# Kernel optimization log

Hardware: AMD Instinct MI355X
Metric: run time of the kernel (lower is better)

The kernel has to match this reference:

```python
import jax, jax.numpy as jnp
import numpy as np
import math

N = 131072   # number of points
C = 32       # embed_dim
K = 19       # num_class
ZD = 16      # z_dim
BN_EPS = 1e-4
SIG_THR = 0.8


def setup_inputs():
    key = jax.random.key(0)
    ks = jax.random.split(key, 16)
    f32 = jnp.float32
    rn = lambda k, s, sc=1.0: jax.random.normal(k, s, dtype=f32) * sc
    return {
        'feat': rn(ks[0], (N, C)),
        'scene_flow': rn(ks[1], (N, 3)),
        'coarse_pred': rn(ks[2], (N, K)),
        'z': rn(ks[3], (ZD,)),
        'select_w1': rn(ks[4], (C, C), 0.2),
        'bn_gamma': jnp.ones((C,), f32),
        'bn_beta': jnp.zeros((C,), f32),
        'bn_mean': jnp.zeros((C,), f32),
        'bn_var': jnp.ones((C,), f32),
        'select_w2': rn(ks[5], (C, 1), 0.2),
        'select_b2': jnp.zeros((1,), f32),
        'wq': rn(ks[6], (C, C), 0.2), 'bq': jnp.zeros((C,), f32),
        'wk': rn(ks[7], (C, C), 0.2), 'bk': jnp.zeros((C,), f32),
        'wv': rn(ks[8], (C, C), 0.2), 'bv': jnp.zeros((C,), f32),
        'wo': rn(ks[9], (C, C), 0.2), 'bo': jnp.zeros((C,), f32),
        'wt': rn(ks[10], (2 * C, C), 0.2), 'bt': jnp.zeros((C,), f32),
        'w_out': rn(ks[11], (C, K), 0.2), 'b_out': jnp.zeros((K,), f32),
        'w_gen': rn(ks[12], (ZD + K + 3, C), 0.2), 'b_gen': jnp.zeros((C,), f32),
    }


def _forward(feat, scene_flow, coarse_pred, z, select_w1, bn_gamma, bn_beta,
             bn_mean, bn_var, select_w2, select_b2, wq, bq, wk, bk, wv, bv,
             wo, bo, wt, bt, w_out, b_out, w_gen, b_gen):
    cp = jax.nn.softmax(coarse_pred, axis=-1)                      # (N, K)
    temp_mask = jnp.any(scene_flow != 0, axis=-1)                  # (N,)
    # select_mlp: Linear(no bias) -> BatchNorm(eval, eps=1e-4) -> ReLU -> Linear -> Sigmoid
    h = (feat @ select_w1 - bn_mean) / jnp.sqrt(bn_var + BN_EPS) * bn_gamma + bn_beta
    h = jnp.maximum(h, 0.0)
    score = jax.nn.sigmoid(h @ select_w2 + select_b2)[:, 0]        # (N,)
    valid = (score < SIG_THR) & temp_mask                          # (N,)
    # cvae stand-in: linear over concat(z, onehot(class), scene_flow) -> (N, K, C)
    wz, wc, ws = w_gen[:ZD], w_gen[ZD:ZD + K], w_gen[ZD + K:]
    gen = (z @ wz + b_gen)[None, None, :] + wc[None, :, :] + (scene_flow @ ws)[:, None, :]
    gen = gen * cp[:, :, None]                                     # scale by softmax prob
    # tiny cross-attention: 1 query per point over K=19 class prototypes
    q = feat @ wq + bq                                             # (N, C)
    k_ = jnp.einsum('nkc,cd->nkd', gen, wk) + bk                   # (N, K, C)
    v_ = jnp.einsum('nkc,cd->nkd', gen, wv) + bv                   # (N, K, C)
    attn = jax.nn.softmax(jnp.einsum('nd,nkd->nk', q, k_) / math.sqrt(C), axis=-1)
    aug = jnp.einsum('nk,nkd->nd', attn, v_) @ wo + bo             # (N, C)
    # scatter-back: invalid points get zeros (equivalent to torch boolean scatter)
    new_feat = jnp.where(valid[:, None], aug, 0.0)
    refine = jnp.concatenate([feat, new_feat], axis=-1) @ wt + bt  # (N, C)
    return refine @ w_out + b_out                                  # (N, K)


def reference(feat, scene_flow, coarse_pred, z, select_w1, bn_gamma, bn_beta,
              bn_mean, bn_var, select_w2, select_b2, wq, bq, wk, bk, wv, bv,
              wo, bo, wt, bt, w_out, b_out, w_gen, b_gen):
    return _forward(feat, scene_flow, coarse_pred, z, select_w1, bn_gamma,
                    bn_beta, bn_mean, bn_var, select_w2, select_b2, wq, bq,
                    wk, bk, wv, bv, wo, bo, wt, bt, w_out, b_out, w_gen, b_gen)
```

## Files before the change

kernel.cpp:

```cpp
#include <hip/hip_runtime.h>

#define NPTS 131072

constexpr int OFF_SW1 = 0;
constexpr int OFF_BNS = 1024;
constexpr int OFF_BNH = 1056;
constexpr int OFF_SW2 = 1088;
constexpr int OFF_B2  = 1120;
constexpr int OFF_QG  = 1121;
constexpr int OFF_QGB = 1729;
constexpr int OFF_QM  = 1748;
constexpr int OFF_QMB = 1844;
constexpr int OFF_QBV = 1847;
constexpr int OFF_QBB = 1879;
constexpr int OFF_A1  = 1880;
constexpr int OFF_GVB = 2488;
constexpr int OFF_MVB = 2849;
constexpr int OFF_CV  = 2906;
constexpr int OFF_BB  = 2925;
constexpr int XG   = 3072;
constexpr int XA2  = 3680;
constexpr int XMK  = 4288;
constexpr int XMV  = 4384;
constexpr int XGK  = 4480;
constexpr int XGV  = 5088;
constexpr int XB   = 5696;

#define CONST_AS __attribute__((address_space(4)))
__device__ __forceinline__ const CONST_AS float* to_const(const float* p) {
    return (const CONST_AS float*)p;
}

__global__ __launch_bounds__(256) void pre_a(
    const float* __restrict__ z,
    const float* __restrict__ sw1,
    const float* __restrict__ bn_gamma, const float* __restrict__ bn_beta,
    const float* __restrict__ bn_mean,  const float* __restrict__ bn_var,
    const float* __restrict__ sw2,      const float* __restrict__ sb2,
    const float* __restrict__ wq, const float* __restrict__ bq,
    const float* __restrict__ wk, const float* __restrict__ bk,
    const float* __restrict__ wv,
    const float* __restrict__ wt, const float* __restrict__ bt,
    const float* __restrict__ wout, const float* __restrict__ bout,
    const float* __restrict__ wgen, const float* __restrict__ bgen,
    float* __restrict__ W)
{
    int i = blockIdx.x * 256 + threadIdx.x;
    if (i < 1024) {
        W[OFF_SW1 + i] = sw1[(i & 31) * 32 + (i >> 5)];
    } else if (i < 1632) {
        int t = i - 1024, e = t / 19, j = t % 19;
        float a1 = 0.f, a2 = 0.f;
        for (int d = 0; d < 32; ++d) {
            float w_ = wout[d*19 + j];
            a1 += wt[e*32 + d] * w_;
            a2 += wt[(32 + e)*32 + d] * w_;
        }
        W[OFF_A1 + t] = a1; W[XA2 + t] = a2;
    } else if (i < 2240) {
        int t = i - 1632, k = t >> 5, e = t & 31;
        float g = bgen[e];
        for (int d = 0; d < 16; ++d) g += z[d] * wgen[d*32 + e];
        W[XG + t] = g + wgen[(16 + k)*32 + e];
    } else if (i < 2336) {
        int t = i - 2240, m = t >> 5, c = t & 31;
        float a = 0.f, b = 0.f;
        for (int e = 0; e < 32; ++e) {
            float wsr = wgen[(35 + m)*32 + e];
            a += wsr * wk[e*32 + c];
            b += wsr * wv[e*32 + c];
        }
        W[XMK + t] = a; W[XMV + t] = b;
    } else if (i < 2368) {
        int t = i - 2336;
        float scale = bn_gamma[t] / sqrtf(bn_var[t] + 1e-4f);
        W[OFF_BNS + t] = scale;
        W[OFF_BNH + t] = bn_beta[t] - bn_mean[t] * scale;
        W[OFF_SW2 + t] = sw2[t];
    } else if (i < 2387) {
        int t = i - 2368;
        float a = bout[t];
        for (int d = 0; d < 32; ++d) a += bt[d] * wout[d*19 + t];
        W[OFF_BB + t] = a;
    } else if (i < 2419) {
        int t = i - 2387;
        float a = 0.f;
        for (int c = 0; c < 32; ++c) a += wq[t*32 + c] * bk[c];
        W[OFF_QBV + t] = a;
    } else if (i == 2419) {
        W[OFF_B2] = sb2[0];
    } else if (i == 2420) {
        float a = 0.f;
        for (int c = 0; c < 32; ++c) a += bq[c] * bk[c];
        W[OFF_QBB] = a;
    }
}

__global__ __launch_bounds__(256) void pre_b(
    const float* __restrict__ wq, const float* __restrict__ bq,
    const float* __restrict__ wk, const float* __restrict__ wv,
    const float* __restrict__ wo,
    float* __restrict__ W)
{
    int i = blockIdx.x * 256 + threadIdx.x;
    if (i < 608) {
        int k = i >> 5, c = i & 31;
        float a = 0.f, b = 0.f;
        for (int e = 0; e < 32; ++e) {
            float g = W[XG + k*32 + e];
            a += g * wk[e*32 + c];
            b += g * wv[e*32 + c];
        }
        W[XGK + i] = a; W[XGV + i] = b;
    } else if (i < 1216) {
        int t = i - 608, c = t / 19, j = t % 19;
        float a = 0.f;
        for (int d = 0; d < 32; ++d) a += wo[c*32 + d] * W[XA2 + d*19 + j];
        W[XB + t] = a;
    } else if (i < 1312) {
        int t = i - 1216, e = t / 3, m = t % 3;
        float a = 0.f;
        for (int c = 0; c < 32; ++c) a += wq[e*32 + c] * W[XMK + m*32 + c];
        W[OFF_QM + t] = a;
    } else if (i < 1315) {
        int m = i - 1312;
        float a = 0.f;
        for (int c = 0; c < 32; ++c) a += bq[c] * W[XMK + m*32 + c];
        W[OFF_QMB + m] = a;
    }
}

__global__ __launch_bounds__(256) void pre_c(
    const float* __restrict__ wq, const float* __restrict__ bq,
    const float* __restrict__ bv, const float* __restrict__ bo,
    float* __restrict__ W)
{
    int i = blockIdx.x * 256 + threadIdx.x;
    if (i < 608) {
        int e = i / 19, k = i % 19;
        float a = 0.f;
        for (int c = 0; c < 32; ++c) a += wq[e*32 + c] * W[XGK + k*32 + c];
        W[OFF_QG + i] = a;
    } else if (i < 627) {
        int k = i - 608;
        float a = 0.f;
        for (int c = 0; c < 32; ++c) a += bq[c] * W[XGK + k*32 + c];
        W[OFF_QGB + k] = a;
    } else if (i < 988) {
        int t = i - 627, k = t / 19, j = t % 19;
        float a = 0.f;
        for (int c = 0; c < 32; ++c) a += W[XGV + k*32 + c] * W[XB + c*19 + j];
        W[OFF_GVB + t] = a;
    } else if (i < 1045) {
        int t = i - 988, m = t / 19, j = t % 19;
        float a = 0.f;
        for (int c = 0; c < 32; ++c) a += W[XMV + m*32 + c] * W[XB + c*19 + j];
        W[OFF_MVB + t] = a;
    } else if (i < 1064) {
        int j = i - 1045;
        float a = 0.f;
        for (int c = 0; c < 32; ++c) a += bv[c] * W[XB + c*19 + j];
        for (int d = 0; d < 32; ++d) a += bo[d] * W[XA2 + d*19 + j];
        W[OFF_CV + j] = a;
    }
}

__global__ __launch_bounds__(256, 1) void main_k(
    const float* __restrict__ feat,
    const float* __restrict__ sflow,
    const float* __restrict__ cpred,
    const float* __restrict__ Wg,
    float* __restrict__ out)
{
    const CONST_AS float* W = to_const(Wg);
    const int n = blockIdx.x * 256 + threadIdx.x;

    float f[32];
    const float4* fp = (const float4*)(feat + (long)n * 32);
#pragma unroll
    for (int g = 0; g < 8; ++g) {
        float4 v = fp[g];
        f[g*4+0] = v.x; f[g*4+1] = v.y; f[g*4+2] = v.z; f[g*4+3] = v.w;
    }

    float s0 = sflow[(long)n*3 + 0];
    float s1 = sflow[(long)n*3 + 1];
    float s2 = sflow[(long)n*3 + 2];
    bool tmask = (s0 != 0.f) | (s1 != 0.f) | (s2 != 0.f);

    float cp[19];
#pragma unroll
    for (int k = 0; k < 19; ++k) cp[k] = cpred[(long)n*19 + k];
    float m1 = cp[0];
#pragma unroll
    for (int k = 1; k < 19; ++k) m1 = fmaxf(m1, cp[k]);
    float sum1 = 0.f;
#pragma unroll
    for (int k = 0; k < 19; ++k) { cp[k] = __expf(cp[k] - m1); sum1 += cp[k]; }
    float r1 = 1.f / sum1;
#pragma unroll
    for (int k = 0; k < 19; ++k) cp[k] *= r1;

    float sacc = W[OFF_B2];
#pragma unroll
    for (int c = 0; c < 32; ++c) {
        float a = 0.f;
#pragma unroll
        for (int e = 0; e < 32; ++e) a = fmaf(f[e], W[OFF_SW1 + c*32 + e], a);
        float h = fmaf(a, W[OFF_BNS + c], W[OFF_BNH + c]);
        h = fmaxf(h, 0.f);
        sacc = fmaf(h, W[OFF_SW2 + c], sacc);
    }
    bool valid = tmask && (sacc < 1.3862943611198906f);

    float qg[19];
#pragma unroll
    for (int k = 0; k < 19; ++k) qg[k] = W[OFF_QGB + k];
    float qm0 = W[OFF_QMB + 0], qm1 = W[OFF_QMB + 1], qm2 = W[OFF_QMB + 2];
    float qb = W[OFF_QBB];
#pragma unroll
    for (int e = 0; e < 32; ++e) {
        float fe = f[e];
#pragma unroll
        for (int k = 0; k < 19; ++k) qg[k] = fmaf(fe, W[OFF_QG + e*19 + k], qg[k]);
        qm0 = fmaf(fe, W[OFF_QM + e*3 + 0], qm0);
        qm1 = fmaf(fe, W[OFF_QM + e*3 + 1], qm1);
        qm2 = fmaf(fe, W[OFF_QM + e*3 + 2], qm2);
        qb  = fmaf(fe, W[OFF_QBV + e], qb);
    }
    float qs = s0*qm0 + s1*qm1 + s2*qm2;

    const float RS = 0.17677669529663687f;
    float l[19];
#pragma unroll
    for (int k = 0; k < 19; ++k) l[k] = fmaf(cp[k], qg[k] + qs, qb) * RS;

    float m2 = l[0];
#pragma unroll
    for (int k = 1; k < 19; ++k) m2 = fmaxf(m2, l[k]);
    float sum2 = 0.f;
#pragma unroll
    for (int k = 0; k < 19; ++k) { l[k] = __expf(l[k] - m2); sum2 += l[k]; }
    float r2 = 1.f / sum2;
    float Sw = 0.f;
#pragma unroll
    for (int k = 0; k < 19; ++k) { l[k] = l[k] * r2 * cp[k]; Sw += l[k]; }

    float o[19];
#pragma unroll
    for (int j = 0; j < 19; ++j) o[j] = W[OFF_BB + j];
#pragma unroll
    for (int e = 0; e < 32; ++e) {
        float fe = f[e];
#pragma unroll
        for (int j = 0; j < 19; ++j) o[j] = fmaf(fe, W[OFF_A1 + e*19 + j], o[j]);
    }

    float a2[19];
#pragma unroll
    for (int j = 0; j < 19; ++j) a2[j] = W[OFF_CV + j];
    float c0 = Sw * s0, c1 = Sw * s1, c2 = Sw * s2;
#pragma unroll
    for (int j = 0; j < 19; ++j) a2[j] = fmaf(c0, W[OFF_MVB + j], a2[j]);
#pragma unroll
    for (int j = 0; j < 19; ++j) a2[j] = fmaf(c1, W[OFF_MVB + 19 + j], a2[j]);
#pragma unroll
    for (int j = 0; j < 19; ++j) a2[j] = fmaf(c2, W[OFF_MVB + 38 + j], a2[j]);
#pragma unroll
    for (int k = 0; k < 19; ++k) {
        float lk = l[k];
#pragma unroll
        for (int j = 0; j < 19; ++j) a2[j] = fmaf(lk, W[OFF_GVB + k*19 + j], a2[j]);
    }

    float vg = valid ? 1.f : 0.f;
    float* op = out + (long)n * 19;
#pragma unroll
    for (int j = 0; j < 19; ++j) op[j] = fmaf(vg, a2[j], o[j]);
}

extern "C" void kernel_launch(void* const* d_in, const int* in_sizes, int n_in,
                              void* d_out, int out_size, void* d_ws, size_t ws_size,
                              hipStream_t stream) {
    const float* feat  = (const float*)d_in[0];
    const float* sflow = (const float*)d_in[1];
    const float* cpred = (const float*)d_in[2];
    const float* z     = (const float*)d_in[3];
    const float* sw1   = (const float*)d_in[4];
    const float* bn_g  = (const float*)d_in[5];
    const float* bn_b  = (const float*)d_in[6];
    const float* bn_m  = (const float*)d_in[7];
    const float* bn_v  = (const float*)d_in[8];
    const float* sw2   = (const float*)d_in[9];
    const float* sb2   = (const float*)d_in[10];
    const float* wq    = (const float*)d_in[11];
    const float* bq    = (const float*)d_in[12];
    const float* wk    = (const float*)d_in[13];
    const float* bk    = (const float*)d_in[14];
    const float* wv    = (const float*)d_in[15];
    const float* bv    = (const float*)d_in[16];
    const float* wo    = (const float*)d_in[17];
    const float* bo    = (const float*)d_in[18];
    const float* wt    = (const float*)d_in[19];
    const float* bt    = (const float*)d_in[20];
    const float* wout  = (const float*)d_in[21];
    const float* bout  = (const float*)d_in[22];
    const float* wgen  = (const float*)d_in[23];
    const float* bgen  = (const float*)d_in[24];

    float* W = (float*)d_ws;

    hipLaunchKernelGGL(pre_a, dim3(10), dim3(256), 0, stream,
                       z, sw1, bn_g, bn_b, bn_m, bn_v, sw2, sb2,
                       wq, bq, wk, bk, wv, wt, bt, wout, bout, wgen, bgen, W);
    hipLaunchKernelGGL(pre_b, dim3(6), dim3(256), 0, stream,
                       wq, bq, wk, wv, wo, W);
    hipLaunchKernelGGL(pre_c, dim3(5), dim3(256), 0, stream,
                       wq, bq, bv, bo, W);

    hipLaunchKernelGGL(main_k, dim3(NPTS / 256), dim3(256), 0, stream,
                       feat, sflow, cpred, W, (float*)d_out);
}
```

Baseline: 165.7 us.

## Stage folded weights in VGPRs and broadcast via readlane instead of scalar loads

Each wavefront now loads the ~2.9K-float folded weight table into 46 VGPRs, one element per lane, and pulls each weight as a uniform value with v_readlane. This replaces the many s_load scalar-cache fetches through the constant address space. The aim is to avoid scalar-memory latency and s_load stalls in the FMA-heavy inner loops. In exchange the kernel uses many more VGPRs and issues a readlane per weight use, which may lengthen the instruction stream or cause spilling.

```diff
diff --git a/kernel.cpp b/kernel.cpp
--- a/kernel.cpp
+++ b/kernel.cpp
@@ -25,11 +25,6 @@
 constexpr int XGK  = 4480;
 constexpr int XGV  = 5088;
 constexpr int XB   = 5696;
-
-#define CONST_AS __attribute__((address_space(4)))
-__device__ __forceinline__ const CONST_AS float* to_const(const float* p) {
-    return (const CONST_AS float*)p;
-}
 
 __global__ __launch_bounds__(256) void pre_a(
     const float* __restrict__ z,
@@ -165,6 +160,11 @@
     }
 }
 
+typedef float vf16 __attribute__((ext_vector_type(16)));
+
+#define TREG(r) ((r) < 16 ? t0[(r)] : ((r) < 32 ? t1[(r)-16] : t2[(r)-32]))
+#define RLW(i) __int_as_float(__builtin_amdgcn_readlane(__float_as_int(TREG((i) >> 6)), (i) & 63))
+
 __global__ __launch_bounds__(256, 1) void main_k(
     const float* __restrict__ feat,
     const float* __restrict__ sflow,
@@ -172,8 +172,17 @@
     const float* __restrict__ Wg,
     float* __restrict__ out)
 {
-    const CONST_AS float* W = to_const(Wg);
     const int n = blockIdx.x * 256 + threadIdx.x;
+    const int lane = threadIdx.x & 63;
+
+    vf16 t0, t1, t2;
+#pragma unroll
+    for (int r = 0; r < 16; ++r) t0[r] = Wg[r * 64 + lane];
+#pragma unroll
+    for (int r = 0; r < 16; ++r) t1[r] = Wg[(16 + r) * 64 + lane];
+#pragma unroll
+    for (int r = 0; r < 14; ++r) t2[r] = Wg[(32 + r) * 64 + lane];
+    t2[14] = 0.f; t2[15] = 0.f;
 
     float f[32];
     const float4* fp = (const float4*)(feat + (long)n * 32);
@@ -201,32 +210,32 @@
 #pragma unroll
     for (int k = 0; k < 19; ++k) cp[k] *= r1;
 
-    float sacc = W[OFF_B2];
+    float sacc = RLW(OFF_B2);
 #pragma unroll
     for (int c = 0; c < 32; ++c) {
         float a = 0.f;
 #pragma unroll
-        for (int e = 0; e < 32; ++e) a = fmaf(f[e], W[OFF_SW1 + c*32 + e], a);
-        float h = fmaf(a, W[OFF_BNS + c], W[OFF_BNH + c]);
+        for (int e = 0; e < 32; ++e) a = fmaf(f[e], RLW(OFF_SW1 + c*32 + e), a);
+        float h = fmaf(a, RLW(OFF_BNS + c), RLW(OFF_BNH + c));
         h = fmaxf(h, 0.f);
-        sacc = fmaf(h, W[OFF_SW2 + c], sacc);
+        sacc = fmaf(h, RLW(OFF_SW2 + c), sacc);
     }
     bool valid = tmask && (sacc < 1.3862943611198906f);
 
     float qg[19];
 #pragma unroll
-    for (int k = 0; k < 19; ++k) qg[k] = W[OFF_QGB + k];
-    float qm0 = W[OFF_QMB + 0], qm1 = W[OFF_QMB + 1], qm2 = W[OFF_QMB + 2];
-    float qb = W[OFF_QBB];
+    for (int k = 0; k < 19; ++k) qg[k] = RLW(OFF_QGB + k);
+    float qm0 = RLW(OFF_QMB + 0), qm1 = RLW(OFF_QMB + 1), qm2 = RLW(OFF_QMB + 2);
+    float qb = RLW(OFF_QBB);
 #pragma unroll
     for (int e = 0; e < 32; ++e) {
         float fe = f[e];
 #pragma unroll
-        for (int k = 0; k < 19; ++k) qg[k] = fmaf(fe, W[OFF_QG + e*19 + k], qg[k]);
-        qm0 = fmaf(fe, W[OFF_QM + e*3 + 0], qm0);
-        qm1 = fmaf(fe, W[OFF_QM + e*3 + 1], qm1);
-        qm2 = fmaf(fe, W[OFF_QM + e*3 + 2], qm2);
-        qb  = fmaf(fe, W[OFF_QBV + e], qb);
+        for (int k = 0; k < 19; ++k) qg[k] = fmaf(fe, RLW(OFF_QG + e*19 + k), qg[k]);
+        qm0 = fmaf(fe, RLW(OFF_QM + e*3 + 0), qm0);
+        qm1 = fmaf(fe, RLW(OFF_QM + e*3 + 1), qm1);
+        qm2 = fmaf(fe, RLW(OFF_QM + e*3 + 2), qm2);
+        qb  = fmaf(fe, RLW(OFF_QBV + e), qb);
     }
     float qs = s0*qm0 + s1*qm1 + s2*qm2;
 
@@ -248,29 +257,29 @@
 
     float o[19];
 #pragma unroll
-    for (int j = 0; j < 19; ++j) o[j] = W[OFF_BB + j];
+    for (int j = 0; j < 19; ++j) o[j] = RLW(OFF_BB + j);
 #pragma unroll
     for (int e = 0; e < 32; ++e) {
         float fe = f[e];
 #pragma unroll
-        for (int j = 0; j < 19; ++j) o[j] = fmaf(fe, W[OFF_A1 + e*19 + j], o[j]);
+        for (int j = 0; j < 19; ++j) o[j] = fmaf(fe, RLW(OFF_A1 + e*19 + j), o[j]);
     }
 
     float a2[19];
 #pragma unroll
-    for (int j = 0; j < 19; ++j) a2[j] = W[OFF_CV + j];
+    for (int j = 0; j < 19; ++j) a2[j] = RLW(OFF_CV + j);
     float c0 = Sw * s0, c1 = Sw * s1, c2 = Sw * s2;
 #pragma unroll
-    for (int j = 0; j < 19; ++j) a2[j] = fmaf(c0, W[OFF_MVB + j], a2[j]);
-#pragma unroll
-    for (int j = 0; j < 19; ++j) a2[j] = fmaf(c1, W[OFF_MVB + 19 + j], a2[j]);
-#pragma unroll
-    for (int j = 0; j < 19; ++j) a2[j] = fmaf(c2, W[OFF_MVB + 38 + j], a2[j]);
+    for (int j = 0; j < 19; ++j) a2[j] = fmaf(c0, RLW(OFF_MVB + j), a2[j]);
+#pragma unroll
+    for (int j = 0; j < 19; ++j) a2[j] = fmaf(c1, RLW(OFF_MVB + 19 + j), a2[j]);
+#pragma unroll
+    for (int j = 0; j < 19; ++j) a2[j] = fmaf(c2, RLW(OFF_MVB + 38 + j), a2[j]);
 #pragma unroll
     for (int k = 0; k < 19; ++k) {
         float lk = l[k];
 #pragma unroll
-        for (int j = 0; j < 19; ++j) a2[j] = fmaf(lk, W[OFF_GVB + k*19 + j], a2[j]);
+        for (int j = 0; j < 19; ++j) a2[j] = fmaf(lk, RLW(OFF_GVB + k*19 + j), a2[j]);
     }
 
     float vg = valid ? 1.f : 0.f;
```

Result: no change. 166.2 us (+0.3%).

## Pack folded weights as bf16 pairs in VGPRs and broadcast via readlane

Applied to the files above, without the earlier changes.

Folded weight tables (QG/A1, GVB, MVB, QM, biases) are rounded to bf16 and packed two per 32-bit word in pre_c. Each wave loads them once into a 15-register vector, and the main kernel pulls values out with readlane, taking the place of scalar constant-memory loads. The QG and A1 loops are fused so one readlane feeds two FMAs. The aim is to cut scalar load traffic and SGPR pressure. The cost is bf16 precision loss on the weights and many readlane/shift instructions.

```diff
diff --git a/kernel.cpp b/kernel.cpp
--- a/kernel.cpp
+++ b/kernel.cpp
@@ -7,17 +7,7 @@
 constexpr int OFF_BNH = 1056;
 constexpr int OFF_SW2 = 1088;
 constexpr int OFF_B2  = 1120;
-constexpr int OFF_QG  = 1121;
-constexpr int OFF_QGB = 1729;
-constexpr int OFF_QM  = 1748;
-constexpr int OFF_QMB = 1844;
-constexpr int OFF_QBV = 1847;
-constexpr int OFF_QBB = 1879;
-constexpr int OFF_A1  = 1880;
-constexpr int OFF_GVB = 2488;
-constexpr int OFF_MVB = 2849;
-constexpr int OFF_CV  = 2906;
-constexpr int OFF_BB  = 2925;
+constexpr int PKB     = 1152;
 constexpr int XG   = 3072;
 constexpr int XA2  = 3680;
 constexpr int XMK  = 4288;
@@ -25,11 +15,27 @@
 constexpr int XGK  = 4480;
 constexpr int XGV  = 5088;
 constexpr int XB   = 5696;
+constexpr int XA1  = 6304;
+constexpr int XBB  = 6912;
+constexpr int XQBV = 6931;
+constexpr int XQBB = 6963;
+constexpr int XQM  = 6964;
+constexpr int XQMB = 7060;
 
 #define CONST_AS __attribute__((address_space(4)))
 __device__ __forceinline__ const CONST_AS float* to_const(const float* p) {
     return (const CONST_AS float*)p;
 }
+
+__device__ __forceinline__ unsigned b16r(float x) {
+    unsigned u = __float_as_uint(x);
+    return (u + 0x7fffu + ((u >> 16) & 1u)) >> 16;
+}
+__device__ __forceinline__ float pk2(float a, float b) {
+    return __uint_as_float(b16r(a) | (b16r(b) << 16));
+}
+__device__ __forceinline__ float plo(unsigned d) { return __uint_as_float(d << 16); }
+__device__ __forceinline__ float phi(unsigned d) { return __uint_as_float(d & 0xffff0000u); }
 
 __global__ __launch_bounds__(256) void pre_a(
     const float* __restrict__ z,
@@ -56,7 +62,7 @@
             a1 += wt[e*32 + d] * w_;
             a2 += wt[(32 + e)*32 + d] * w_;
         }
-        W[OFF_A1 + t] = a1; W[XA2 + t] = a2;
+        W[XA1 + t] = a1; W[XA2 + t] = a2;
     } else if (i < 2240) {
         int t = i - 1632, k = t >> 5, e = t & 31;
         float g = bgen[e];
@@ -81,18 +87,18 @@
         int t = i - 2368;
         float a = bout[t];
         for (int d = 0; d < 32; ++d) a += bt[d] * wout[d*19 + t];
-        W[OFF_BB + t] = a;
+        W[XBB + t] = a;
     } else if (i < 2419) {
         int t = i - 2387;
         float a = 0.f;
         for (int c = 0; c < 32; ++c) a += wq[t*32 + c] * bk[c];
-        W[OFF_QBV + t] = a;
+        W[XQBV + t] = a;
     } else if (i == 2419) {
         W[OFF_B2] = sb2[0];
     } else if (i == 2420) {
         float a = 0.f;
         for (int c = 0; c < 32; ++c) a += bq[c] * bk[c];
-        W[OFF_QBB] = a;
+        W[XQBB] = a;
     }
 }
 
@@ -121,12 +127,12 @@
         int t = i - 1216, e = t / 3, m = t % 3;
         float a = 0.f;
         for (int c = 0; c < 32; ++c) a += wq[e*32 + c] * W[XMK + m*32 + c];
-        W[OFF_QM + t] = a;
+        W[XQM + t] = a;
     } else if (i < 1315) {
         int m = i - 1312;
         float a = 0.f;
         for (int c = 0; c < 32; ++c) a += bq[c] * W[XMK + m*32 + c];
-        W[OFF_QMB + m] = a;
+        W[XQMB + m] = a;
     }
 }
 
@@ -135,35 +141,54 @@
     const float* __restrict__ bv, const float* __restrict__ bo,
     float* __restrict__ W)
 {
-    int i = blockIdx.x * 256 + threadIdx.x;
-    if (i < 608) {
-        int e = i / 19, k = i % 19;
-        float a = 0.f;
-        for (int c = 0; c < 32; ++c) a += wq[e*32 + c] * W[XGK + k*32 + c];
-        W[OFF_QG + i] = a;
-    } else if (i < 627) {
-        int k = i - 608;
-        float a = 0.f;
-        for (int c = 0; c < 32; ++c) a += bq[c] * W[XGK + k*32 + c];
-        W[OFF_QGB + k] = a;
-    } else if (i < 988) {
-        int t = i - 627, k = t / 19, j = t % 19;
-        float a = 0.f;
-        for (int c = 0; c < 32; ++c) a += W[XGV + k*32 + c] * W[XB + c*19 + j];
-        W[OFF_GVB + t] = a;
-    } else if (i < 1045) {
-        int t = i - 988, m = t / 19, j = t % 19;
-        float a = 0.f;
-        for (int c = 0; c < 32; ++c) a += W[XMV + m*32 + c] * W[XB + c*19 + j];
-        W[OFF_MVB + t] = a;
-    } else if (i < 1064) {
-        int j = i - 1045;
-        float a = 0.f;
-        for (int c = 0; c < 32; ++c) a += bv[c] * W[XB + c*19 + j];
-        for (int d = 0; d < 32; ++d) a += bo[d] * W[XA2 + d*19 + j];
-        W[OFF_CV + j] = a;
-    }
-}
+    int p = blockIdx.x * 256 + threadIdx.x;
+    if (p < 608) {
+        int e = p / 19, k = p % 19;
+        float qg = 0.f;
+        for (int c = 0; c < 32; ++c) qg += wq[e*32 + c] * W[XGK + k*32 + c];
+        W[PKB + p] = pk2(qg, W[XA1 + p]);
+    } else if (p < 798) {
+        int t = p - 608, k = t / 10, h = t % 10, j0 = 2*h;
+        float g0 = 0.f, g1 = 0.f;
+        for (int c = 0; c < 32; ++c) g0 += W[XGV + k*32 + c] * W[XB + c*19 + j0];
+        if (j0 + 1 < 19)
+            for (int c = 0; c < 32; ++c) g1 += W[XGV + k*32 + c] * W[XB + c*19 + j0 + 1];
+        W[PKB + p] = pk2(g0, g1);
+    } else if (p < 828) {
+        int t = p - 798, m = t / 10, h = t % 10, j0 = 2*h;
+        float g0 = 0.f, g1 = 0.f;
+        for (int c = 0; c < 32; ++c) g0 += W[XMV + m*32 + c] * W[XB + c*19 + j0];
+        if (j0 + 1 < 19)
+            for (int c = 0; c < 32; ++c) g1 += W[XMV + m*32 + c] * W[XB + c*19 + j0 + 1];
+        W[PKB + p] = pk2(g0, g1);
+    } else if (p < 892) {
+        int t = p - 828, e = t >> 1;
+        if ((t & 1) == 0) W[PKB + p] = pk2(W[XQM + e*3 + 0], W[XQM + e*3 + 1]);
+        else              W[PKB + p] = pk2(W[XQM + e*3 + 2], W[XQBV + e]);
+    } else if (p < 911) {
+        int k = p - 892;
+        float qgb = 0.f;
+        for (int c = 0; c < 32; ++c) qgb += bq[c] * W[XGK + k*32 + c];
+        W[PKB + p] = pk2(qgb, W[XBB + k]);
+    } else if (p < 921) {
+        int h = p - 911, j0 = 2*h;
+        float c0 = 0.f, c1 = 0.f;
+        for (int c = 0; c < 32; ++c) c0 += bv[c] * W[XB + c*19 + j0];
+        for (int d = 0; d < 32; ++d) c0 += bo[d] * W[XA2 + d*19 + j0];
+        if (j0 + 1 < 19) {
+            for (int c = 0; c < 32; ++c) c1 += bv[c] * W[XB + c*19 + j0 + 1];
+            for (int d = 0; d < 32; ++d) c1 += bo[d] * W[XA2 + d*19 + j0 + 1];
+        }
+        W[PKB + p] = pk2(c0, c1);
+    } else if (p == 921) {
+        W[PKB + p] = pk2(W[XQMB + 0], W[XQMB + 1]);
+    } else if (p == 922) {
+        W[PKB + p] = pk2(W[XQMB + 2], W[XQBB]);
+    }
+}
+
+typedef float vf16 __attribute__((ext_vector_type(16)));
+#define RLP(p) ((unsigned)__builtin_amdgcn_readlane(__float_as_int(tp[(p) >> 6]), (p) & 63))
 
 __global__ __launch_bounds__(256, 1) void main_k(
     const float* __restrict__ feat,
@@ -174,6 +199,12 @@
 {
     const CONST_AS float* W = to_const(Wg);
     const int n = blockIdx.x * 256 + threadIdx.x;
+    const int lane = threadIdx.x & 63;
+
+    vf16 tp;
+#pragma unroll
+    for (int r = 0; r < 15; ++r) tp[r] = Wg[PKB + r * 64 + lane];
+    tp[15] = 0.f;
 
     float f[32];
     const float4* fp = (const float4*)(feat + (long)n * 32);
@@ -182,7 +213,6 @@
         float4 v = fp[g];
         f[g*4+0] = v.x; f[g*4+1] = v.y; f[g*4+2] = v.z; f[g*4+3] = v.w;
     }
-
     float s0 = sflow[(long)n*3 + 0];
     float s1 = sflow[(long)n*3 + 1];
     float s2 = sflow[(long)n*3 + 2];
@@ -213,20 +243,23 @@
     }
     bool valid = tmask && (sacc < 1.3862943611198906f);
 
-    float qg[19];
-#pragma unroll
-    for (int k = 0; k < 19; ++k) qg[k] = W[OFF_QGB + k];
-    float qm0 = W[OFF_QMB + 0], qm1 = W[OFF_QMB + 1], qm2 = W[OFF_QMB + 2];
-    float qb = W[OFF_QBB];
+    float qg[19], o[19];
+#pragma unroll
+    for (int k = 0; k < 19; ++k) { unsigned d = RLP(892 + k); qg[k] = plo(d); o[k] = phi(d); }
+    float qm0, qm1, qm2, qb;
+    { unsigned d = RLP(921); qm0 = plo(d); qm1 = phi(d); }
+    { unsigned d = RLP(922); qm2 = plo(d); qb  = phi(d); }
 #pragma unroll
     for (int e = 0; e < 32; ++e) {
         float fe = f[e];
 #pragma unroll
-        for (int k = 0; k < 19; ++k) qg[k] = fmaf(fe, W[OFF_QG + e*19 + k], qg[k]);
-        qm0 = fmaf(fe, W[OFF_QM + e*3 + 0], qm0);
-        qm1 = fmaf(fe, W[OFF_QM + e*3 + 1], qm1);
-        qm2 = fmaf(fe, W[OFF_QM + e*3 + 2], qm2);
-        qb  = fmaf(fe, W[OFF_QBV + e], qb);
+        for (int k = 0; k < 19; ++k) {
+            unsigned d = RLP(e*19 + k);
+            qg[k] = fmaf(fe, plo(d), qg[k]);
+            o[k]  = fmaf(fe, phi(d), o[k]);
+        }
+        { unsigned d = RLP(828 + 2*e);     qm0 = fmaf(fe, plo(d), qm0); qm1 = fmaf(fe, phi(d), qm1); }
+        { unsigned d = RLP(828 + 2*e + 1); qm2 = fmaf(fe, plo(d), qm2); qb  = fmaf(fe, phi(d), qb); }
     }
     float qs = s0*qm0 + s1*qm1 + s2*qm2;
 
@@ -246,31 +279,29 @@
 #pragma unroll
     for (int k = 0; k < 19; ++k) { l[k] = l[k] * r2 * cp[k]; Sw += l[k]; }
 
-    float o[19];
-#pragma unroll
-    for (int j = 0; j < 19; ++j) o[j] = W[OFF_BB + j];
-#pragma unroll
-    for (int e = 0; e < 32; ++e) {
-        float fe = f[e];
-#pragma unroll
-        for (int j = 0; j < 19; ++j) o[j] = fmaf(fe, W[OFF_A1 + e*19 + j], o[j]);
-    }
-
-    float a2[19];
-#pragma unroll
-    for (int j = 0; j < 19; ++j) a2[j] = W[OFF_CV + j];
-    float c0 = Sw * s0, c1 = Sw * s1, c2 = Sw * s2;
-#pragma unroll
-    for (int j = 0; j < 19; ++j) a2[j] = fmaf(c0, W[OFF_MVB + j], a2[j]);
-#pragma unroll
-    for (int j = 0; j < 19; ++j) a2[j] = fmaf(c1, W[OFF_MVB + 19 + j], a2[j]);
-#pragma unroll
-    for (int j = 0; j < 19; ++j) a2[j] = fmaf(c2, W[OFF_MVB + 38 + j], a2[j]);
+    float a2[20];
+#pragma unroll
+    for (int h = 0; h < 10; ++h) { unsigned d = RLP(911 + h); a2[2*h] = plo(d); a2[2*h+1] = phi(d); }
+    float cms[3] = { Sw * s0, Sw * s1, Sw * s2 };
+#pragma unroll
+    for (int m = 0; m < 3; ++m) {
+        float cm = cms[m];
+#pragma unroll
+        for (int h = 0; h < 10; ++h) {
+            unsigned d = RLP(798 + m*10 + h);
+            a2[2*h]   = fmaf(cm, plo(d), a2[2*h]);
+            a2[2*h+1] = fmaf(cm, phi(d), a2[2*h+1]);
+        }
+    }
 #pragma unroll
     for (int k = 0; k < 19; ++k) {
         float lk = l[k];
 #pragma unroll
-        for (int j = 0; j < 19; ++j) a2[j] = fmaf(lk, W[OFF_GVB + k*19 + j], a2[j]);
+        for (int h = 0; h < 10; ++h) {
+            unsigned d = RLP(608 + k*10 + h);
+            a2[2*h]   = fmaf(lk, plo(d), a2[2*h]);
+            a2[2*h+1] = fmaf(lk, phi(d), a2[2*h+1]);
+        }
     }
 
     float vg = valid ? 1.f : 0.f;
@@ -315,7 +346,7 @@
                        wq, bq, wk, bk, wv, wt, bt, wout, bout, wgen, bgen, W);
     hipLaunchKernelGGL(pre_b, dim3(6), dim3(256), 0, stream,
                        wq, bq, wk, wv, wo, W);
-    hipLaunchKernelGGL(pre_c, dim3(5), dim3(256), 0, stream,
+    hipLaunchKernelGGL(pre_c, dim3(4), dim3(256), 0, stream,
                        wq, bq, bv, bo, W);
 
     hipLaunchKernelGGL(main_k, dim3(NPTS / 256), dim3(256), 0, stream,
```

New measurement: 161.5 us. -2.5%, faster.
